# Kernel tuning notes

Measured on AMD Instinct MI355X. Metric: run time of the kernel, lower is better.

## Reference

```python
import jax, jax.numpy as jnp
import numpy as np
from jax import lax

B = 32768  # number of 5x5 patches processed in a batch
NUM_MID = 6  # middle 25->25 conv layers (layers 1..6 of 8)
NUM_W = 6    # predicted kernel weights per pixel


def _conv(x, w, b, pad):
    # x: [B,C,H,W], w: [O,I,kh,kw]
    y = lax.conv_general_dilated(x, w, (1, 1), pad,
                                 dimension_numbers=('NCHW', 'OIHW', 'NCHW'))
    return y + b[None, :, None, None]


def setup_inputs() -> dict:
    key = jax.random.key(0)
    ks = jax.random.split(key, 10)
    s = 0.1
    inp = {
        'input': jax.random.normal(ks[0], (B, 8, 5, 5), dtype=jnp.float32),
        'w0': jax.random.normal(ks[1], (25, 8, 3, 3), dtype=jnp.float32) * s,
        'b0': jax.random.normal(ks[2], (25,), dtype=jnp.float32) * s,
        'wmid': jax.random.normal(ks[3], (NUM_MID, 25, 25, 3, 3), dtype=jnp.float32) * s,
        'bmid': jax.random.normal(ks[4], (NUM_MID, 25), dtype=jnp.float32) * s,
        'wlast': jax.random.normal(ks[5], (NUM_W, 25, 3, 3), dtype=jnp.float32) * s,
        'blast': jax.random.normal(ks[6], (NUM_W,), dtype=jnp.float32) * s,
        'wpost': jax.random.normal(ks[7], (3 * NUM_W, 3, 5, 5), dtype=jnp.float32) * s,
        'bpost': jax.random.normal(ks[8], (3 * NUM_W,), dtype=jnp.float32) * s,
    }
    return inp


def reference(input, w0, b0, wmid, bmid, wlast, blast, wpost, bpost):
    # 8-layer tiny CNN predicting per-pixel softmax weights over NUM_W kernels
    h = jax.nn.relu(_conv(input, w0, b0, 'SAME'))
    for i in range(NUM_MID):  # fixed small layer count
        h = jax.nn.relu(_conv(h, wmid[i], bmid[i], 'SAME'))
    h = _conv(h, wlast, blast, 'SAME')            # [B, NUM_W, 5, 5]
    norm_w = jax.nn.softmax(h, axis=1)            # softmax over weight channels
    # postconv: 5x5 valid conv on first 3 channels -> [B, 3*NUM_W, 1, 1] -> [B,3,NUM_W]
    colors = _conv(input[:, 0:3], wpost, bpost, 'VALID').reshape(B, 3, NUM_W)
    # per-pixel matmul: filtered[:,y,x] = colors @ norm_w[:,y,x]
    filtered = jnp.einsum('bcw,bwyx->bcyx', colors, norm_w)  # [B,3,5,5]
    return filtered
```

## Files before the change

kernel.cpp:

```cpp
#include <hip/hip_runtime.h>
#include <hip/hip_bf16.h>
#include <stdint.h>


typedef short bf16x8 __attribute__((ext_vector_type(8)));
typedef float f32x4  __attribute__((ext_vector_type(4)));

#define WSB_N     73728
#define WSF_BYTE  147456
#define WSF_BALL  0
#define WSF_WPOST 256
#define WSF_BPOST 1606
#define WSF_N     1624

__device__ __forceinline__ float b2f(unsigned short u) {
  union { unsigned int u; float f; } v; v.u = ((unsigned int)u) << 16; return v.f;
}
__device__ __forceinline__ unsigned short f2b(float f) {
  union { float f; unsigned int u; } v; v.f = f;
  unsigned int r = v.u + 0x7fffu + ((v.u >> 16) & 1u);
  return (unsigned short)(r >> 16);
}
__device__ __forceinline__ unsigned int pk2(float lo, float hi) {
  __hip_bfloat162 h = __float22bfloat162_rn(make_float2(lo, hi));
  union { __hip_bfloat162 h; unsigned int u; } v; v.h = h; return v.u;
}
__device__ __forceinline__ bool sniff_is_f32(const void* w0raw) {
  const unsigned short* q = (const unsigned short*)w0raw;
  int hits = 0;
  #pragma unroll
  for (int i = 0; i < 64; ++i) {
    unsigned int e = (q[i] >> 7) & 0xFFu;
    if (e >= 130u) ++hits;
  }
  return hits > 0;
}
__device__ __forceinline__ float ldw(const void* p, long idx, bool f32) {
  return f32 ? ((const float*)p)[idx] : b2f(((const unsigned short*)p)[idx]);
}
__device__ __forceinline__ int kperm(int m) {
  return (m < 16) ? ((m >> 2) * 8 + (m & 3))
                  : (((m - 16) >> 2) * 8 + 4 + (m & 3));
}

__global__ void prep_weights(const void* __restrict__ w0,
                             const void* __restrict__ b0,
                             const void* __restrict__ wm,
                             const void* __restrict__ bm,
                             const void* __restrict__ wl,
                             const void* __restrict__ bl,
                             const void* __restrict__ wp,
                             const void* __restrict__ bp,
                             unsigned short* __restrict__ wsb,
                             float* __restrict__ wsf) {
  const bool f32 = sniff_is_f32(w0);
  int e = blockIdx.x * blockDim.x + threadIdx.x;
  if (e < WSB_N) {
    int l = e / 9216, r = e % 9216, t = r / 1024, r2 = r % 1024;
    int o = r2 >> 5, c = r2 & 31;
    float v = 0.f;
    if (l < 7) {
      int co = kperm(o);
      if (co < 25) {
        if (l == 0) { if (c < 8)  v = ldw(w0, (co * 8 + c) * 9 + t, f32); }
        else        { if (c < 25) v = ldw(wm, (((l - 1) * 25 + co) * 25 + c) * 9 + t, f32); }
      }
    } else {
      if (o < 6 && c < 25) v = ldw(wl, (o * 25 + c) * 9 + t, f32);
    }
    wsb[e] = f2b(v);
  } else {
    int q = e - WSB_N;
    if (q < 256) {
      int l = q >> 5, m = q & 31;
      float v = 0.f;
      if (l < 7) {
        int co = kperm(m);
        if (co < 25) v = (l == 0) ? ldw(b0, co, f32) : ldw(bm, (l - 1) * 25 + co, f32);
      } else {
        if (m < 6) v = ldw(bl, m, f32);
      }
      wsf[WSF_BALL + q] = v;
    } else if (q < 256 + 1350) {
      wsf[WSF_WPOST + (q - 256)] = ldw(wp, q - 256, f32);
    } else if (q < WSF_N) {
      wsf[WSF_BPOST + (q - 1606)] = ldw(bp, q - 1606, f32);
    }
  }
}

__global__ __launch_bounds__(64)
__attribute__((amdgpu_waves_per_eu(2, 2)))
void pcnn_mfma(
    const void* __restrict__ inp,
    const void* __restrict__ w0raw,
    const unsigned short* __restrict__ wsb,
    const float* __restrict__ wsf,
    void* __restrict__ out) {
  __shared__ __align__(16) unsigned char u9600[9600];
  __shared__ float in3[1200];
  __shared__ float colb[288];
  short* stage = (short*)u9600;
  float* smb   = (float*)u9600;

  const bool f32m = sniff_is_f32(w0raw);
  const int lane = threadIdx.x;
  const int col  = lane & 15;
  const int quad = lane >> 4;
  const long g   = blockIdx.x;

  #pragma unroll 1
  for (int c0 = 0; c0 < 3200; c0 += 1600) {
    float v[25];
    #pragma unroll
    for (int j = 0; j < 25; ++j)
      v[j] = ldw(inp, g * 3200 + c0 + j * 64 + lane, f32m);
    #pragma unroll
    for (int j = 0; j < 25; ++j) {
      const int e = c0 + j * 64 + lane;
      int b = e / 200, r = e % 200, c = r / 25, px = r % 25;
      stage[px * 128 + b * 8 + c] = f2b(v[j]);
      if (c < 3) in3[b * 75 + c * 25 + px] = v[j];
    }
  }
  __asm__ volatile("s_waitcnt lgkmcnt(0)" ::: "memory");

  bf16x8 X[25], Y[25];
  #pragma unroll
  for (int p = 0; p < 25; ++p) {
    union { bf16x8 v; uint4 q4; } t;
    t.q4 = make_uint4(0u, 0u, 0u, 0u);
    if (quad == 0) t.q4 = *(const uint4*)(stage + p * 128 + col * 8);
    X[p] = t.v;
  }

  auto conv = [&](const bf16x8 (&in)[25], bf16x8 (&outp)[25], int l) {
    const unsigned short* WA = wsb + l * 9216;
    bf16x8 A0[9], A1[9];
    #pragma unroll
    for (int t = 0; t < 9; ++t) {
      A0[t] = *(const bf16x8*)(WA + t * 1024 + col * 32 + quad * 8);
      A1[t] = *(const bf16x8*)(WA + t * 1024 + (16 + col) * 32 + quad * 8);
    }
    const f32x4 bias0 = *(const f32x4*)(wsf + WSF_BALL + l * 32 + quad * 4);
    const f32x4 bias1 = *(const f32x4*)(wsf + WSF_BALL + l * 32 + 16 + quad * 4);
    #pragma unroll
    for (int p = 0; p < 25; ++p) {
      const int py = p / 5, pxx = p % 5;
      f32x4 a0e = bias0, a1e = bias1;
      f32x4 a0o = {0.f, 0.f, 0.f, 0.f}, a1o = {0.f, 0.f, 0.f, 0.f};
      #pragma unroll
      for (int dy = -1; dy <= 1; ++dy)
        #pragma unroll
        for (int dx = -1; dx <= 1; ++dx)
          if ((unsigned)(py + dy) < 5u && (unsigned)(pxx + dx) < 5u) {
            const int t = (dy + 1) * 3 + (dx + 1);
            const int q = p + dy * 5 + dx;
            if (t & 1) {
              a0o = __builtin_amdgcn_mfma_f32_16x16x32_bf16(A0[t], in[q], a0o, 0, 0, 0);
              a1o = __builtin_amdgcn_mfma_f32_16x16x32_bf16(A1[t], in[q], a1o, 0, 0, 0);
            } else {
              a0e = __builtin_amdgcn_mfma_f32_16x16x32_bf16(A0[t], in[q], a0e, 0, 0, 0);
              a1e = __builtin_amdgcn_mfma_f32_16x16x32_bf16(A1[t], in[q], a1e, 0, 0, 0);
            }
          }
      union { bf16x8 v; unsigned int uu[4]; } nb;
      nb.uu[0] = pk2(fmaxf(a0e[0] + a0o[0], 0.f), fmaxf(a0e[1] + a0o[1], 0.f));
      nb.uu[1] = pk2(fmaxf(a0e[2] + a0o[2], 0.f), fmaxf(a0e[3] + a0o[3], 0.f));
      nb.uu[2] = pk2(fmaxf(a1e[0] + a1o[0], 0.f), fmaxf(a1e[1] + a1o[1], 0.f));
      nb.uu[3] = pk2(fmaxf(a1e[2] + a1o[2], 0.f), fmaxf(a1e[3] + a1o[3], 0.f));
      outp[p] = nb.v;
    }
  };

  conv(X, Y, 0);
  #pragma unroll 1
  for (int i = 0; i < 3; ++i) {
    conv(Y, X, 2 * i + 1);
    conv(X, Y, 2 * i + 2);
  }

  {
    const unsigned short* WA = wsb + 7 * 9216;
    bf16x8 A[9];
    #pragma unroll
    for (int t = 0; t < 9; ++t)
      A[t] = *(const bf16x8*)(WA + t * 1024 + col * 32 + quad * 8);
    const f32x4 biasl = *(const f32x4*)(wsf + WSF_BALL + 7 * 32 + quad * 4);
    #pragma unroll
    for (int p = 0; p < 25; ++p) {
      const int py = p / 5, pxx = p % 5;
      f32x4 ae = biasl, ao = {0.f, 0.f, 0.f, 0.f};
      #pragma unroll
      for (int dy = -1; dy <= 1; ++dy)
        #pragma unroll
        for (int dx = -1; dx <= 1; ++dx)
          if ((unsigned)(py + dy) < 5u && (unsigned)(pxx + dx) < 5u) {
            const int t = (dy + 1) * 3 + (dx + 1);
            const int q = p + dy * 5 + dx;
            if (t & 1)
              ao = __builtin_amdgcn_mfma_f32_16x16x32_bf16(A[t], Y[q], ao, 0, 0, 0);
            else
              ae = __builtin_amdgcn_mfma_f32_16x16x32_bf16(A[t], Y[q], ae, 0, 0, 0);
          }
      f32x4 a;
      a[0] = ae[0] + ao[0]; a[1] = ae[1] + ao[1];
      a[2] = ae[2] + ao[2]; a[3] = ae[3] + ao[3];
      float l4 = __shfl_xor(a[0], 16);
      float l5 = __shfl_xor(a[1], 16);
      if (quad == 0) {
        float m = fmaxf(fmaxf(fmaxf(a[0], a[1]), fmaxf(a[2], a[3])), fmaxf(l4, l5));
        float e0 = __expf(a[0] - m), e1 = __expf(a[1] - m), e2 = __expf(a[2] - m);
        float e3 = __expf(a[3] - m), e4 = __expf(l4 - m), e5 = __expf(l5 - m);
        float inv = 1.f / (e0 + e1 + e2 + e3 + e4 + e5);
        float* sp = smb + p * 96 + col * 6;
        sp[0] = e0 * inv; sp[1] = e1 * inv; sp[2] = e2 * inv;
        sp[3] = e3 * inv; sp[4] = e4 * inv; sp[5] = e5 * inv;
      }
    }
  }
  __asm__ volatile("s_waitcnt lgkmcnt(0)" ::: "memory");

  for (int j = lane; j < 288; j += 64) {
    int b = j / 18, oc = j % 18;
    float s = wsf[WSF_BPOST + oc];
    #pragma unroll
    for (int ic = 0; ic < 3; ++ic)
      #pragma unroll
      for (int px = 0; px < 25; ++px)
        s = fmaf(wsf[WSF_WPOST + (oc * 3 + ic) * 25 + px], in3[b * 75 + ic * 25 + px], s);
    colb[b * 18 + oc] = s;
  }
  __asm__ volatile("s_waitcnt lgkmcnt(0)" ::: "memory");

  for (int e = lane; e < 1200; e += 64) {
    int b = e / 75, r = e % 75, c = r / 25, p = r % 25;
    float v = 0.f;
    #pragma unroll
    for (int w = 0; w < 6; ++w)
      v = fmaf(colb[b * 18 + c * 6 + w], smb[p * 96 + b * 6 + w], v);
    const long oidx = g * 1200 + e;
    if (f32m) ((float*)out)[oidx] = v;
    else      ((unsigned short*)out)[oidx] = f2b(v);
  }
}

extern "C" void kernel_launch(void* const* d_in, const int* in_sizes, int n_in,
                              void* d_out, int out_size, void* d_ws, size_t ws_size,
                              hipStream_t stream) {
  unsigned short* wsb = (unsigned short*)d_ws;
  float* wsf = (float*)((char*)d_ws + WSF_BYTE);
  const int B = in_sizes[0] / 200;

  const int prep_n = WSB_N + WSF_N;
  prep_weights<<<(prep_n + 255) / 256, 256, 0, stream>>>(
      d_in[1], d_in[2], d_in[3], d_in[4], d_in[5], d_in[6], d_in[7], d_in[8],
      wsb, wsf);
  pcnn_mfma<<<B / 16, 64, 0, stream>>>(d_in[0], d_in[1], wsb, wsf, d_out);
}
```

Measured before the change: 170.1 us.

## Compute postconv colors with split-bf16 MFMA instead of scalar FMA loop

Replaces the scalar 5x5 valid postconv (1350 FMAs per output read from global/LDS) with MFMA calls. Inputs and weights are split into bf16 hi/lo parts so the products keep near-fp32 accuracy. Postconv weights are packed into unused rows of the last-layer weight block during prep, and the LDS layout is reorganised. It also wraps the conv MFMA chains in s_setprio to favour matrix issue. The cost is extra LDS traffic, zero-fill work and register pressure for the preloaded weight fragments.

```diff
diff --git a/kernel.cpp b/kernel.cpp
--- a/kernel.cpp
+++ b/kernel.cpp
@@ -7,10 +7,10 @@
 typedef float f32x4  __attribute__((ext_vector_type(4)));
 
 #define WSB_N     73728
+#define WSB_EMB   6144
 #define WSF_BYTE  147456
 #define WSF_BALL  0
-#define WSF_WPOST 256
-#define WSF_BPOST 1606
+#define WSF_BP32  256
 #define WSF_N     1624
 
 __device__ __forceinline__ float b2f(unsigned short u) {
@@ -58,6 +58,7 @@
   if (e < WSB_N) {
     int l = e / 9216, r = e % 9216, t = r / 1024, r2 = r % 1024;
     int o = r2 >> 5, c = r2 & 31;
+    if (l == 7 && o >= 6) return;
     float v = 0.f;
     if (l < 7) {
       int co = kperm(o);
@@ -66,11 +67,22 @@
         else        { if (c < 25) v = ldw(wm, (((l - 1) * 25 + co) * 25 + c) * 9 + t, f32); }
       }
     } else {
-      if (o < 6 && c < 25) v = ldw(wl, (o * 25 + c) * 9 + t, f32);
+      if (c < 25) v = ldw(wl, (o * 25 + c) * 9 + t, f32);
     }
     wsb[e] = f2b(v);
+  } else if (e < WSB_N + WSB_EMB) {
+    int idx = e - WSB_N;
+    int hl = idx / 3072, rem = idx % 3072;
+    int chunk = rem / 1024, r2 = rem % 1024;
+    int o = r2 >> 5, k = r2 & 31;
+    float w = (o < 18 && k < 25) ? ldw(wp, (o * 3 + chunk) * 25 + k, f32) : 0.f;
+    unsigned short hi = f2b(w);
+    unsigned short val = hl ? f2b(w - b2f(hi)) : hi;
+    int rowidx = hl * 96 + chunk * 32 + o;
+    int t = rowidx / 26, rr = 6 + rowidx % 26;
+    wsb[7 * 9216 + t * 1024 + rr * 32 + k] = val;
   } else {
-    int q = e - WSB_N;
+    int q = e - WSB_N - WSB_EMB;
     if (q < 256) {
       int l = q >> 5, m = q & 31;
       float v = 0.f;
@@ -81,10 +93,9 @@
         if (m < 6) v = ldw(bl, m, f32);
       }
       wsf[WSF_BALL + q] = v;
-    } else if (q < 256 + 1350) {
-      wsf[WSF_WPOST + (q - 256)] = ldw(wp, q - 256, f32);
-    } else if (q < WSF_N) {
-      wsf[WSF_BPOST + (q - 1606)] = ldw(bp, q - 1606, f32);
+    } else if (q < 288) {
+      int oc = q - 256;
+      wsf[WSF_BP32 + oc] = (oc < 18) ? ldw(bp, oc, f32) : 0.f;
     }
   }
 }
@@ -97,11 +108,11 @@
     const unsigned short* __restrict__ wsb,
     const float* __restrict__ wsf,
     void* __restrict__ out) {
-  __shared__ __align__(16) unsigned char u9600[9600];
-  __shared__ float in3[1200];
-  __shared__ float colb[288];
-  short* stage = (short*)u9600;
-  float* smb   = (float*)u9600;
+  __shared__ __align__(16) unsigned char pool[13696];
+  short* stage = (short*)pool;
+  short* inpk  = (short*)(pool + 6400);
+  float* colb  = (float*)(pool + 12544);
+  float* smb   = (float*)pool;
 
   const bool f32m = sniff_is_f32(w0raw);
   const int lane = threadIdx.x;
@@ -109,21 +120,59 @@
   const int quad = lane >> 4;
   const long g   = blockIdx.x;
 
+  bf16x8 WC[2][3][2];
+  #pragma unroll
+  for (int hl = 0; hl < 2; ++hl)
+    #pragma unroll
+    for (int ch = 0; ch < 3; ++ch)
+      #pragma unroll
+      for (int hf = 0; hf < 2; ++hf) {
+        const int rowidx = hl * 96 + ch * 32 + hf * 16 + col;
+        const int t = rowidx / 26, rr = 6 + rowidx % 26;
+        WC[hl][ch][hf] = *(const bf16x8*)(wsb + 7 * 9216 + t * 1024 + rr * 32 + quad * 8);
+      }
+  f32x4 c0 = *(const f32x4*)(wsf + WSF_BP32 + quad * 4);
+  f32x4 c1 = *(const f32x4*)(wsf + WSF_BP32 + 16 + quad * 4);
+
+  for (int i = lane; i < 672; i += 64) {
+    int s = 25 + i % 7, rest = i / 7;
+    inpk[rest * 32 + s] = 0;
+  }
+
   #pragma unroll 1
-  for (int c0 = 0; c0 < 3200; c0 += 1600) {
+  for (int c0i = 0; c0i < 3200; c0i += 1600) {
     float v[25];
     #pragma unroll
     for (int j = 0; j < 25; ++j)
-      v[j] = ldw(inp, g * 3200 + c0 + j * 64 + lane, f32m);
+      v[j] = ldw(inp, g * 3200 + c0i + j * 64 + lane, f32m);
     #pragma unroll
     for (int j = 0; j < 25; ++j) {
-      const int e = c0 + j * 64 + lane;
+      const int e = c0i + j * 64 + lane;
       int b = e / 200, r = e % 200, c = r / 25, px = r % 25;
-      stage[px * 128 + b * 8 + c] = f2b(v[j]);
-      if (c < 3) in3[b * 75 + c * 25 + px] = v[j];
+      unsigned short hi = f2b(v[j]);
+      stage[px * 128 + b * 8 + c] = hi;
+      if (c < 3) {
+        inpk[((0 * 3 + c) * 16 + b) * 32 + px] = hi;
+        inpk[((1 * 3 + c) * 16 + b) * 32 + px] = f2b(v[j] - b2f(hi));
+      }
     }
   }
   __asm__ volatile("s_waitcnt lgkmcnt(0)" ::: "memory");
+
+  #pragma unroll
+  for (int ch = 0; ch < 3; ++ch) {
+    bf16x8 Bhi = *(const bf16x8*)(inpk + ((0 * 3 + ch) * 16 + col) * 32 + quad * 8);
+    bf16x8 Blo = *(const bf16x8*)(inpk + ((1 * 3 + ch) * 16 + col) * 32 + quad * 8);
+    c0 = __builtin_amdgcn_mfma_f32_16x16x32_bf16(WC[0][ch][0], Bhi, c0, 0, 0, 0);
+    c0 = __builtin_amdgcn_mfma_f32_16x16x32_bf16(WC[0][ch][0], Blo, c0, 0, 0, 0);
+    c0 = __builtin_amdgcn_mfma_f32_16x16x32_bf16(WC[1][ch][0], Bhi, c0, 0, 0, 0);
+    c1 = __builtin_amdgcn_mfma_f32_16x16x32_bf16(WC[0][ch][1], Bhi, c1, 0, 0, 0);
+    c1 = __builtin_amdgcn_mfma_f32_16x16x32_bf16(WC[0][ch][1], Blo, c1, 0, 0, 0);
+    c1 = __builtin_amdgcn_mfma_f32_16x16x32_bf16(WC[1][ch][1], Bhi, c1, 0, 0, 0);
+  }
+  #pragma unroll
+  for (int r = 0; r < 4; ++r) colb[col * 18 + quad * 4 + r] = c0[r];
+  if (quad == 0) { colb[col * 18 + 16] = c1[0]; colb[col * 18 + 17] = c1[1]; }
 
   bf16x8 X[25], Y[25];
   #pragma unroll
@@ -149,6 +198,7 @@
       const int py = p / 5, pxx = p % 5;
       f32x4 a0e = bias0, a1e = bias1;
       f32x4 a0o = {0.f, 0.f, 0.f, 0.f}, a1o = {0.f, 0.f, 0.f, 0.f};
+      __builtin_amdgcn_s_setprio(1);
       #pragma unroll
       for (int dy = -1; dy <= 1; ++dy)
         #pragma unroll
@@ -164,6 +214,7 @@
               a1e = __builtin_amdgcn_mfma_f32_16x16x32_bf16(A1[t], in[q], a1e, 0, 0, 0);
             }
           }
+      __builtin_amdgcn_s_setprio(0);
       union { bf16x8 v; unsigned int uu[4]; } nb;
       nb.uu[0] = pk2(fmaxf(a0e[0] + a0o[0], 0.f), fmaxf(a0e[1] + a0o[1], 0.f));
       nb.uu[1] = pk2(fmaxf(a0e[2] + a0o[2], 0.f), fmaxf(a0e[3] + a0o[3], 0.f));
@@ -191,6 +242,7 @@
     for (int p = 0; p < 25; ++p) {
       const int py = p / 5, pxx = p % 5;
       f32x4 ae = biasl, ao = {0.f, 0.f, 0.f, 0.f};
+      __builtin_amdgcn_s_setprio(1);
       #pragma unroll
       for (int dy = -1; dy <= 1; ++dy)
         #pragma unroll
@@ -203,6 +255,7 @@
             else
               ae = __builtin_amdgcn_mfma_f32_16x16x32_bf16(A[t], Y[q], ae, 0, 0, 0);
           }
+      __builtin_amdgcn_s_setprio(0);
       f32x4 a;
       a[0] = ae[0] + ao[0]; a[1] = ae[1] + ao[1];
       a[2] = ae[2] + ao[2]; a[3] = ae[3] + ao[3];
@@ -221,18 +274,6 @@
   }
   __asm__ volatile("s_waitcnt lgkmcnt(0)" ::: "memory");
 
-  for (int j = lane; j < 288; j += 64) {
-    int b = j / 18, oc = j % 18;
-    float s = wsf[WSF_BPOST + oc];
-    #pragma unroll
-    for (int ic = 0; ic < 3; ++ic)
-      #pragma unroll
-      for (int px = 0; px < 25; ++px)
-        s = fmaf(wsf[WSF_WPOST + (oc * 3 + ic) * 25 + px], in3[b * 75 + ic * 25 + px], s);
-    colb[b * 18 + oc] = s;
-  }
-  __asm__ volatile("s_waitcnt lgkmcnt(0)" ::: "memory");
-
   for (int e = lane; e < 1200; e += 64) {
     int b = e / 75, r = e % 75, c = r / 25, p = r % 25;
     float v = 0.f;
@@ -252,7 +293,7 @@
   float* wsf = (float*)((char*)d_ws + WSF_BYTE);
   const int B = in_sizes[0] / 200;
 
-  const int prep_n = WSB_N + WSF_N;
+  const int prep_n = WSB_N + WSB_EMB + 288;
   prep_weights<<<(prep_n + 255) / 256, 256, 0, stream>>>(
       d_in[1], d_in[2], d_in[3], d_in[4], d_in[5], d_in[6], d_in[7], d_in[8],
       wsb, wsf);
```

Result: faster. 159.4 us (-6.3%).
